# Optimization experiments

Measured on AMD Instinct MI355X. Metric: run time of the kernel, lower is better.

## Reference

```python
import jax, jax.numpy as jnp
import numpy as np
from functools import partial

H = 768          # hidden_size (bert-base)
S = 256          # seq_len, forced by pool Linear(256*H -> H)
V = 30522        # vocab_size
NUM_TAGS = 2
B = 32


def _lstm_layer(x, w_ih, w_hh, b_ih, b_hh):
    # x: (B, S, I); torch weight layout: w_ih (4H, I), w_hh (4H, H), gate order i,f,g,o
    b, _, _ = x.shape
    h0 = jnp.zeros((b, H), x.dtype)
    c0 = jnp.zeros((b, H), x.dtype)
    bias = b_ih + b_hh

    def step(carry, xt):
        h, c = carry
        gates = xt @ w_ih.T + h @ w_hh.T + bias          # (B, 4H)
        i, f, g, o = jnp.split(gates, 4, axis=-1)
        i = jax.nn.sigmoid(i)
        f = jax.nn.sigmoid(f)
        g = jnp.tanh(g)
        o = jax.nn.sigmoid(o)
        c = f * c + i * g
        h = o * jnp.tanh(c)
        return (h, c), h

    _, hs = jax.lax.scan(step, (h0, c0), x.transpose(1, 0, 2))  # hs: (S, B, H)
    return hs.transpose(1, 0, 2)


def setup_inputs() -> dict:
    key = jax.random.key(0)
    ks = jax.random.split(key, 16)
    sc = 0.02
    inp = {
        "input_ids": jax.random.randint(ks[0], (B, S), 0, V, dtype=jnp.int32),
        "attention_mask": jnp.ones((B, S), jnp.int32),
        "token_type_ids": jnp.zeros((B, S), jnp.int32),
        "seq_label": jax.random.randint(ks[1], (B, NUM_TAGS), 0, 2, dtype=jnp.int32),
        "entity_ids": jax.random.randint(ks[2], (B, S), 0, 2, dtype=jnp.int32),
        "embed_table": jax.random.normal(ks[3], (V, H), jnp.float32) * sc,
        "w_ih0": jax.random.normal(ks[4], (4 * H, H), jnp.float32) * sc,
        "w_hh0": jax.random.normal(ks[5], (4 * H, H), jnp.float32) * sc,
        "b_ih0": jnp.zeros((4 * H,), jnp.float32),
        "b_hh0": jnp.zeros((4 * H,), jnp.float32),
        "w_ih1": jax.random.normal(ks[6], (4 * H, H), jnp.float32) * sc,
        "w_hh1": jax.random.normal(ks[7], (4 * H, H), jnp.float32) * sc,
        "b_ih1": jnp.zeros((4 * H,), jnp.float32),
        "b_hh1": jnp.zeros((4 * H,), jnp.float32),
        "pool_w": jax.random.normal(ks[8], (S * H, H), jnp.float32) * 0.002,
        "pool_b": jnp.zeros((H,), jnp.float32),
        "lin_w": jax.random.normal(ks[9], (H, NUM_TAGS), jnp.float32) * sc,
        "lin_b": jnp.zeros((NUM_TAGS,), jnp.float32),
    }
    return inp


def reference(input_ids, attention_mask, token_type_ids, seq_label, entity_ids,
              embed_table, w_ih0, w_hh0, b_ih0, b_hh0, w_ih1, w_hh1, b_ih1, b_hh1,
              pool_w, pool_b, lin_w, lin_b):
    x = embed_table[input_ids]                              # (B, S, H)
    out = _lstm_layer(x, w_ih0, w_hh0, b_ih0, b_hh0)        # layer 1
    out = _lstm_layer(out, w_ih1, w_hh1, b_ih1, b_hh1)      # layer 2 -> (B, S, H)

    seq_out = out.reshape(out.shape[0], -1) @ pool_w + pool_b   # (B, H)

    # batched version of the per-sample loop:
    # entity_out = tokens * (entity_ids == 1); concat seq_out row; global max over tokens
    mask = (entity_ids == 1).astype(out.dtype)[:, :, None]      # (B, S, 1)
    entity_out = out * mask                                     # (B, S, H)
    batch_out = jnp.maximum(entity_out.max(axis=1), seq_out)    # adaptive_max_pool1d(size=1)

    logits = batch_out @ lin_w + lin_b                          # (B, num_tags)

    # BCEWithLogitsLoss (dropout in eval mode = identity), numerically stable
    y = seq_label.astype(logits.dtype)
    loss = jnp.mean(jnp.maximum(logits, 0) - logits * y + jnp.log1p(jnp.exp(-jnp.abs(logits))))
    return (loss, logits)
```

## Files before the change

### kernel.cpp

```cpp
#include <hip/hip_runtime.h>
#include <hip/hip_bf16.h>
#include <stdint.h>

constexpr int Hh  = 768;
constexpr int Ss  = 256;
constexpr int Bb  = 32;
constexpr int G4  = 4 * Hh;
constexpr int MR  = Bb * Ss;
constexpr int NWGL = 96;
constexpr int UPW8 = Hh / NWGL;
constexpr int LCW  = 4 * UPW8;
constexpr int WPAD = Hh + 8;
constexpr int PB   = Bb + 2;
constexpr int KH   = Hh / 2;
constexpr int CPT  = 256;

typedef short bf16x8 __attribute__((ext_vector_type(8)));
typedef float f32x4  __attribute__((ext_vector_type(4)));
typedef float f32x2  __attribute__((ext_vector_type(2)));

__device__ __forceinline__ unsigned short f2bf(float f) {
  union { float f; uint32_t u; } v; v.f = f;
  uint32_t u = v.u;
  return (unsigned short)((u + 0x7FFFu + ((u >> 16) & 1u)) >> 16);
}
__device__ __forceinline__ float bf2f(unsigned short h) {
  union { uint32_t u; float f; } v; v.u = ((uint32_t)h) << 16; return v.f;
}

__global__ __launch_bounds__(256) void k_embed(const int* __restrict__ ids,
                                               const float* __restrict__ table,
                                               unsigned short* __restrict__ x_bf) {
  int row = blockIdx.x;
  int id  = ids[row];
  const float* src = table + (size_t)id * Hh;
  unsigned short* dst = x_bf + (size_t)row * Hh;
  for (int j = threadIdx.x; j < Hh; j += 256) dst[j] = f2bf(src[j]);
}

__global__ __launch_bounds__(256) void k_cast(const float* __restrict__ src,
                                              unsigned short* __restrict__ dst, int n4) {
  int i = blockIdx.x * 256 + threadIdx.x;
  if (i < n4) {
    float4 v = ((const float4*)src)[i];
    uint2 o;
    o.x = (uint32_t)f2bf(v.x) | ((uint32_t)f2bf(v.y) << 16);
    o.y = (uint32_t)f2bf(v.z) | ((uint32_t)f2bf(v.w) << 16);
    ((uint2*)dst)[i] = o;
  }
}

__global__ __launch_bounds__(256) void k_gemm_bt(const unsigned short* __restrict__ A,
                                                 const unsigned short* __restrict__ Bw,
                                                 unsigned short* __restrict__ g2,
                                                 const float* __restrict__ bias1,
                                                 const float* __restrict__ bias2,
                                                 int M, int N, int K) {
  constexpr int BM = 128, BN = 128, BK = 64;
  __shared__ unsigned short Asm[BM * BK];
  __shared__ unsigned short Bsm[BN * BK];
  const int tid = threadIdx.x, lane = tid & 63, wave = tid >> 6;
  const int m0 = blockIdx.x * BM, n0 = blockIdx.y * BN;
  const int wm = (wave & 1) * 64, wn = (wave >> 1) * 64;

  f32x4 acc[4][4];
  #pragma unroll
  for (int a = 0; a < 4; ++a)
    #pragma unroll
    for (int b = 0; b < 4; ++b) acc[a][b] = (f32x4){0.f, 0.f, 0.f, 0.f};

  const int nk = K / BK;
  bf16x8 ar[4], br[4];
  #pragma unroll
  for (int r = 0; r < 4; ++r) {
    int fb = r * 4096 + tid * 16;
    int row = fb >> 7;
    int kb  = (fb >> 4) & 7;
    ar[r] = *(const bf16x8*)(A  + (size_t)(m0 + row) * K + kb * 8);
    br[r] = *(const bf16x8*)(Bw + (size_t)(n0 + row) * K + kb * 8);
  }
  for (int it = 0; it < nk; ++it) {
    __syncthreads();
    #pragma unroll
    for (int r = 0; r < 4; ++r) {
      int fb = r * 4096 + tid * 16;
      int row = fb >> 7;
      int kb  = (fb >> 4) & 7;
      int sb  = kb ^ (row & 7);
      *(bf16x8*)((char*)Asm + row * 128 + sb * 16) = ar[r];
      *(bf16x8*)((char*)Bsm + row * 128 + sb * 16) = br[r];
    }
    __syncthreads();
    if (it + 1 < nk) {
      int k0 = (it + 1) * BK;
      #pragma unroll
      for (int r = 0; r < 4; ++r) {
        int fb = r * 4096 + tid * 16;
        int row = fb >> 7;
        int kb  = (fb >> 4) & 7;
        ar[r] = *(const bf16x8*)(A  + (size_t)(m0 + row) * K + k0 + kb * 8);
        br[r] = *(const bf16x8*)(Bw + (size_t)(n0 + row) * K + k0 + kb * 8);
      }
    }
    #pragma unroll
    for (int kk = 0; kk < 2; ++kk) {
      bf16x8 af[4], bfr[4];
      #pragma unroll
      for (int mi = 0; mi < 4; ++mi) {
        int row = wm + mi * 16 + (lane & 15);
        int kb  = kk * 4 + (lane >> 4);
        int sb  = kb ^ (row & 7);
        af[mi] = *(const bf16x8*)((const char*)Asm + row * 128 + sb * 16);
      }
      #pragma unroll
      for (int ni = 0; ni < 4; ++ni) {
        int row = wn + ni * 16 + (lane & 15);
        int kb  = kk * 4 + (lane >> 4);
        int sb  = kb ^ (row & 7);
        bfr[ni] = *(const bf16x8*)((const char*)Bsm + row * 128 + sb * 16);
      }
      #pragma unroll
      for (int mi = 0; mi < 4; ++mi)
        #pragma unroll
        for (int ni = 0; ni < 4; ++ni)
          acc[mi][ni] = __builtin_amdgcn_mfma_f32_16x16x32_bf16(af[mi], bfr[ni], acc[mi][ni], 0, 0, 0);
    }
  }
  #pragma unroll
  for (int mi = 0; mi < 4; ++mi)
    #pragma unroll
    for (int ni = 0; ni < 4; ++ni)
      #pragma unroll
      for (int r = 0; r < 4; ++r) {
        int row = m0 + wm + mi * 16 + (lane >> 4) * 4 + r;
        int n   = n0 + wn + ni * 16 + (lane & 15);
        int bb = row >> 8, ss = row & 255;
        int gi = n / Hh, u = n - gi * Hh;
        int wg = u >> 3, lc = gi * 8 + (u & 7);
        float v = acc[mi][ni][r] + bias1[n] + bias2[n];
        g2[(((size_t)ss * NWGL + wg) * Bb + bb) * LCW + lc] = f2bf(v);
      }
}

__global__ __launch_bounds__(128) void k_lstm2(
    const unsigned short* __restrict__ g2,
    const unsigned short* __restrict__ w_hh0b,
    const unsigned short* __restrict__ w_ih1b,
    const unsigned short* __restrict__ w_hh1b,
    const float* __restrict__ b_ih1,
    const float* __restrict__ b_hh1,
    unsigned short* __restrict__ hseq1,
    unsigned short* __restrict__ hseq2,
    unsigned int* __restrict__ sync) {
  __shared__ __align__(16) unsigned short Whh[LCW * WPAD];
  __shared__ __align__(16) unsigned short Wih[LCW * WPAD];
  __shared__ __align__(16) unsigned short hbuf[2][16][8];

  const int wgid = blockIdx.x;
  const int tid = threadIdx.x;
  const int lane = tid & 63, w = tid >> 6;
  unsigned int* cnt1 = sync;
  unsigned int* cnt2 = sync + Ss * CPT;

  const int layer = wgid >= NWGL;
  const int wg = layer ? wgid - NWGL : wgid;
  const int u0 = wg * UPW8;
  const int bkt = wg & 15;

  {
    const unsigned short* src = layer ? w_hh1b : w_hh0b;
    for (int cch = tid; cch < LCW * 96; cch += 128) {
      int row = cch / 96, kc = cch - row * 96;
      int gi = row >> 3, u = row & 7;
      *(bf16x8*)&Whh[row * WPAD + kc * 8] =
          *(const bf16x8*)(src + (size_t)(gi * Hh + u0 + u) * Hh + kc * 8);
    }
    if (layer) {
      for (int cch = tid; cch < LCW * 96; cch += 128) {
        int row = cch / 96, kc = cch - row * 96;
        int gi = row >> 3, u = row & 7;
        *(bf16x8*)&Wih[row * WPAD + kc * 8] =
            *(const bf16x8*)(w_ih1b + (size_t)(gi * Hh + u0 + u) * Hh + kc * 8);
      }
    }
  }
  __syncthreads();

  const int l15 = lane & 15, kq = lane >> 4;
  const int brow = w * 16 + l15;
  const bool lo8 = (l15 < 8);

  const float k1 = lo8 ? 2.f : 1.f;
  const float m1 = lo8 ? 2.f : 1.f;
  const float d1 = lo8 ? -1.f : 0.f;

  float bl[2] = {0.f, 0.f};
  if (layer) {
    #pragma unroll
    for (int nt = 0; nt < 2; ++nt) {
      int c = nt * 16 + l15;
      int gcol = (c >> 3) * Hh + u0 + (c & 7);
      bl[nt] = b_ih1[gcol] + b_hh1[gcol];
    }
  }

  unsigned short gc[2][4];
  if (!layer) {
    const unsigned short* grow = g2 + ((size_t)0 * NWGL + wg) * (Bb * LCW);
    #pragma unroll
    for (int nt = 0; nt < 2; ++nt)
      #pragma unroll
      for (int r = 0; r < 4; ++r)
        gc[nt][r] = grow[(w * 16 + kq * 4 + r) * LCW + nt * 16 + l15];
  }
  float cc[4] = {0.f, 0.f, 0.f, 0.f};
  unsigned short* hout = layer ? hseq2 : hseq1;
  unsigned int* mycnt = layer ? cnt2 : cnt1;

  for (int t = 0; t < Ss; ++t) {
    if (layer) {
      if (w == 0) {
        const unsigned int* b1 = cnt1 + (size_t)t * CPT;
        const unsigned int* b2 = cnt2 + (size_t)(t - 1) * CPT;
        const bool needOwn = (t > 0);
        for (;;) {
          unsigned v = 12;
          if (lane < 16)
            v = __hip_atomic_load(b1 + lane * 16, __ATOMIC_RELAXED, __HIP_MEMORY_SCOPE_AGENT);
          else if (lane < 32 && needOwn)
            v = __hip_atomic_load(b2 + (lane - 16) * 16, __ATOMIC_RELAXED, __HIP_MEMORY_SCOPE_AGENT);
          if (__all(v >= 12u)) break;
          __builtin_amdgcn_s_sleep(1);
        }
      }
      __syncthreads();
      asm volatile("" ::: "memory");
    } else if (t > 0) {
      if (w == 0) {
        const unsigned int* b1 = cnt1 + (size_t)(t - 1) * CPT;
        for (;;) {
          unsigned v = 12;
          if (lane < 16)
            v = __hip_atomic_load(b1 + lane * 16, __ATOMIC_RELAXED, __HIP_MEMORY_SCOPE_AGENT);
          if (__all(v >= 12u)) break;
          __builtin_amdgcn_s_sleep(1);
        }
      }
      __syncthreads();
      asm volatile("" ::: "memory");
    }

    f32x4 aI[2][2], aW[2][2];
    #pragma unroll
    for (int nt = 0; nt < 2; ++nt) {
      aI[nt][0] = (f32x4){0.f,0.f,0.f,0.f}; aI[nt][1] = (f32x4){0.f,0.f,0.f,0.f};
      aW[nt][0] = (f32x4){0.f,0.f,0.f,0.f}; aW[nt][1] = (f32x4){0.f,0.f,0.f,0.f};
    }
    if (layer) {
      const unsigned short* ap = hseq1 + ((size_t)t * Bb + brow) * Hh + kq * 8;
      bf16x8 areg[24];
      #pragma unroll
      for (int kk = 0; kk < 24; ++kk) areg[kk] = *(const bf16x8*)(ap + kk * 32);
      #pragma unroll
      for (int nt = 0; nt < 2; ++nt) {
        const int c = nt * 16 + l15;
        #pragma unroll
        for (int kk = 0; kk < 24; ++kk) {
          bf16x8 bfr = *(const bf16x8*)&Wih[c * WPAD + kk * 32 + kq * 8];
          aI[nt][kk & 1] = __builtin_amdgcn_mfma_f32_16x16x32_bf16(areg[kk], bfr, aI[nt][kk & 1], 0, 0, 0);
        }
      }
    }
    if (t > 0) {
      const unsigned short* ap = hout + ((size_t)(t - 1) * Bb + brow) * Hh + kq * 8;
      bf16x8 areg[24];
      #pragma unroll
      for (int kk = 0; kk < 24; ++kk) areg[kk] = *(const bf16x8*)(ap + kk * 32);
      #pragma unroll
      for (int nt = 0; nt < 2; ++nt) {
        const int c = nt * 16 + l15;
        #pragma unroll
        for (int kk = 0; kk < 24; ++kk) {
          bf16x8 bfr = *(const bf16x8*)&Whh[c * WPAD + kk * 32 + kq * 8];
          aW[nt][kk & 1] = __builtin_amdgcn_mfma_f32_16x16x32_bf16(areg[kk], bfr, aW[nt][kk & 1], 0, 0, 0);
        }
      }
    }

    float act0[4], act1[4];
    #pragma unroll
    for (int r = 0; r < 4; ++r) {
      float v0 = aI[0][0][r] + aI[0][1][r] + aW[0][0][r] + aW[0][1][r]
               + (layer ? bl[0] : bf2f(gc[0][r]));
      act0[r] = 1.f / (1.f + __expf(-v0));
      float v1 = aI[1][0][r] + aI[1][1][r] + aW[1][0][r] + aW[1][1][r]
               + (layer ? bl[1] : bf2f(gc[1][r]));
      act1[r] = m1 / (1.f + __expf(-k1 * v1)) + d1;
    }

    #pragma unroll
    for (int r = 0; r < 4; ++r) {
      float p0 = __shfl_xor(act0[r], 8);
      float p1 = __shfl_xor(act1[r], 8);
      float iv = lo8 ? act0[r] : p0;
      float fv = lo8 ? p0 : act0[r];
      float gv = lo8 ? act1[r] : p1;
      float ov = lo8 ? p1 : act1[r];
      float cn = fv * cc[r] + iv * gv;
      cc[r] = cn;
      float e = __expf(-2.f * cn);
      float hv = ov * (1.f - e) / (1.f + e);
      if (lo8) hbuf[w][kq * 4 + r][l15] = f2bf(hv);
    }
    asm volatile("s_waitcnt lgkmcnt(0)" ::: "memory");

    if (lane < 16) {
      const unsigned long long* hb = (const unsigned long long*)&hbuf[w][lane][0];
      unsigned long long x0 = hb[0], x1 = hb[1];
      unsigned long long* hp =
          (unsigned long long*)(hout + ((size_t)t * Bb + (w * 16 + lane)) * Hh + u0);
      __hip_atomic_store(hp + 0, x0, __ATOMIC_RELAXED, __HIP_MEMORY_SCOPE_AGENT);
      __hip_atomic_store(hp + 1, x1, __ATOMIC_RELAXED, __HIP_MEMORY_SCOPE_AGENT);
    }
    asm volatile("s_waitcnt vmcnt(0)" ::: "memory");
    if (lane == 0) {
      unsigned int* cp = mycnt + (size_t)t * CPT + bkt * 16;
      (void)__hip_atomic_fetch_add(cp, 1u, __ATOMIC_RELAXED, __HIP_MEMORY_SCOPE_AGENT);
    }

    if (!layer && t + 1 < Ss) {
      const unsigned short* grow = g2 + ((size_t)(t + 1) * NWGL + wg) * (Bb * LCW);
      #pragma unroll
      for (int nt = 0; nt < 2; ++nt)
        #pragma unroll
        for (int r = 0; r < 4; ++r)
          gc[nt][r] = grow[(w * 16 + kq * 4 + r) * LCW + nt * 16 + l15];
    }
  }
}

__global__ __launch_bounds__(256) void k_pool_partial(const unsigned short* __restrict__ hseq2,
                                                      const float* __restrict__ pw,
                                                      float* __restrict__ partial) {
  __shared__ unsigned short osm[KH * PB];
  const int tid = threadIdx.x;
  const int s = blockIdx.x, half = blockIdx.y;
  const int k0 = half * KH;
  for (int b = 0; b < Bb; ++b) {
    const unsigned short* src = hseq2 + ((size_t)s * Bb + b) * Hh + k0;
    for (int k = tid; k < KH; k += 256) osm[k * PB + b] = src[k];
  }
  __syncthreads();
  f32x2 acc[16][3];
  #pragma unroll
  for (int bp = 0; bp < 16; ++bp)
    #pragma unroll
    for (int j = 0; j < 3; ++j) acc[bp][j] = (f32x2){0.f, 0.f};
  const float* pbase = pw + (size_t)s * Hh * Hh + (size_t)k0 * Hh;
  #pragma unroll 4
  for (int k = 0; k < KH; ++k) {
    float w0 = pbase[(size_t)k * Hh + tid];
    float w1 = pbase[(size_t)k * Hh + 256 + tid];
    float w2 = pbase[(size_t)k * Hh + 512 + tid];
    const uint32_t* orow = (const uint32_t*)&osm[k * PB];
    #pragma unroll
    for (int bp = 0; bp < 16; ++bp) {
      uint32_t pv = orow[bp];
      f32x2 ov;
      ov.x = __uint_as_float(pv << 16);
      ov.y = __uint_as_float(pv & 0xffff0000u);
      acc[bp][0] += ov * w0;
      acc[bp][1] += ov * w1;
      acc[bp][2] += ov * w2;
    }
  }
  float* pout = partial + (size_t)(s * 2 + half) * (Bb * Hh);
  #pragma unroll
  for (int bp = 0; bp < 16; ++bp)
    #pragma unroll
    for (int j = 0; j < 3; ++j) {
      pout[(size_t)(bp * 2 + 0) * Hh + j * 256 + tid] = acc[bp][j].x;
      pout[(size_t)(bp * 2 + 1) * Hh + j * 256 + tid] = acc[bp][j].y;
    }
}

__global__ __launch_bounds__(256) void k_pool_reduce(const float* __restrict__ partial,
                                                     const float* __restrict__ pool_b,
                                                     float* __restrict__ seq_out) {
  int i = blockIdx.x * 256 + threadIdx.x;
  float acc = pool_b[i % Hh];
  #pragma unroll 8
  for (int t = 0; t < 2 * Ss; ++t) acc += partial[(size_t)t * (Bb * Hh) + i];
  seq_out[i] = acc;
}

__global__ __launch_bounds__(256) void k_entity_logits(const unsigned short* __restrict__ hseq2,
                                                       const float* __restrict__ seq_out,
                                                       const int* __restrict__ entity_ids,
                                                       const float* __restrict__ lin_w,
                                                       const float* __restrict__ lin_b,
                                                       float* __restrict__ logits_ws,
                                                       float* __restrict__ dlogits) {
  const int b = blockIdx.x, tid = threadIdx.x;
  float m0 = -1e30f, m1 = -1e30f, m2 = -1e30f;
  for (int s = 0; s < Ss; ++s) {
    bool e = entity_ids[b * Ss + s] == 1;
    const unsigned short* row = hseq2 + ((size_t)s * Bb + b) * Hh;
    float v0 = bf2f(row[tid]);
    float v1 = bf2f(row[256 + tid]);
    float v2 = bf2f(row[512 + tid]);
    v0 = e ? v0 : 0.f; v1 = e ? v1 : 0.f; v2 = e ? v2 : 0.f;
    m0 = fmaxf(m0, v0); m1 = fmaxf(m1, v1); m2 = fmaxf(m2, v2);
  }
  __shared__ float red[512];
  float p0 = 0.f, p1 = 0.f;
  float mm[3] = {m0, m1, m2};
  #pragma unroll
  for (int j = 0; j < 3; ++j) {
    int n = j * 256 + tid;
    float bo = fmaxf(mm[j], seq_out[b * Hh + n]);
    p0 += bo * lin_w[n * 2 + 0];
    p1 += bo * lin_w[n * 2 + 1];
  }
  red[tid] = p0; red[256 + tid] = p1;
  __syncthreads();
  for (int off = 128; off > 0; off >>= 1) {
    if (tid < off) { red[tid] += red[tid + off]; red[256 + tid] += red[256 + tid + off]; }
    __syncthreads();
  }
  if (tid == 0) {
    float l0 = red[0] + lin_b[0], l1 = red[256] + lin_b[1];
    logits_ws[b * 2] = l0; logits_ws[b * 2 + 1] = l1;
    dlogits[b * 2] = l0;  dlogits[b * 2 + 1] = l1;
  }
}

__global__ void k_loss(const float* __restrict__ logits, const int* __restrict__ lab,
                       float* __restrict__ dout) {
  __shared__ float red[64];
  int i = threadIdx.x;
  float l = logits[i];
  float y = (float)lab[i];
  red[i] = fmaxf(l, 0.f) - l * y + log1pf(__expf(-fabsf(l)));
  __syncthreads();
  for (int off = 32; off > 0; off >>= 1) {
    if (i < off) red[i] += red[i + off];
    __syncthreads();
  }
  if (i == 0) dout[0] = red[0] * (1.f / 64.f);
}

extern "C" void kernel_launch(void* const* d_in, const int* in_sizes, int n_in,
                              void* d_out, int out_size, void* d_ws, size_t ws_size,
                              hipStream_t stream) {
  const int*   input_ids  = (const int*)d_in[0];
  const int*   seq_label  = (const int*)d_in[3];
  const int*   entity_ids = (const int*)d_in[4];
  const float* embed      = (const float*)d_in[5];
  const float* w_ih0      = (const float*)d_in[6];
  const float* w_hh0      = (const float*)d_in[7];
  const float* b_ih0      = (const float*)d_in[8];
  const float* b_hh0      = (const float*)d_in[9];
  const float* w_ih1      = (const float*)d_in[10];
  const float* w_hh1      = (const float*)d_in[11];
  const float* b_ih1      = (const float*)d_in[12];
  const float* b_hh1      = (const float*)d_in[13];
  const float* pool_w     = (const float*)d_in[14];
  const float* pool_b     = (const float*)d_in[15];
  const float* lin_w      = (const float*)d_in[16];
  const float* lin_b      = (const float*)d_in[17];
  float* out = (float*)d_out;

  const size_t SZ_XO = (size_t)Bb * Ss * Hh * 2;
  const size_t SZ_W  = (size_t)G4 * Hh * 2;
  const size_t SZ_G  = (size_t)Bb * Ss * G4 * 2;
  const size_t SZ_SY = (size_t)2 * Ss * CPT * 4;
  char* ws = (char*)d_ws;
  size_t off = 0;
  unsigned short* x_bf   = (unsigned short*)(ws + off); off += SZ_XO;
  unsigned short* wb_ih0 = (unsigned short*)(ws + off); off += SZ_W;
  unsigned short* wb_hh0 = (unsigned short*)(ws + off); off += SZ_W;
  unsigned short* wb_ih1 = (unsigned short*)(ws + off); off += SZ_W;
  unsigned short* wb_hh1 = (unsigned short*)(ws + off); off += SZ_W;
  unsigned short* g2     = (unsigned short*)(ws + off); off += SZ_G;
  unsigned short* hseq1  = (unsigned short*)(ws + off); off += SZ_XO;
  unsigned short* hseq2  = (unsigned short*)(ws + off); off += SZ_XO;
  float*          seq_out= (float*)(ws + off);          off += (size_t)Bb * Hh * 4;
  float*          logits = (float*)(ws + off);          off += 1024;
  unsigned int*   syncb  = (unsigned int*)(ws + off);   off += SZ_SY;
  float*          partial = (float*)ws;

  hipMemsetAsync(syncb, 0, SZ_SY, stream);

  k_embed<<<Bb * Ss, 256, 0, stream>>>(input_ids, embed, x_bf);
  int n4 = (G4 * Hh) / 4;
  int cgrid = (n4 + 255) / 256;
  k_cast<<<cgrid, 256, 0, stream>>>(w_ih0, wb_ih0, n4);
  k_cast<<<cgrid, 256, 0, stream>>>(w_hh0, wb_hh0, n4);
  k_cast<<<cgrid, 256, 0, stream>>>(w_ih1, wb_ih1, n4);
  k_cast<<<cgrid, 256, 0, stream>>>(w_hh1, wb_hh1, n4);

  dim3 ggrid(MR / 128, G4 / 128);
  k_gemm_bt<<<ggrid, 256, 0, stream>>>(x_bf, wb_ih0, g2, b_ih0, b_hh0, MR, G4, Hh);

  k_lstm2<<<2 * NWGL, 128, 0, stream>>>(g2, wb_hh0, wb_ih1, wb_hh1,
                                        b_ih1, b_hh1, hseq1, hseq2, syncb);

  dim3 pgrid(Ss, 2);
  k_pool_partial<<<pgrid, 256, 0, stream>>>(hseq2, pool_w, partial);
  k_pool_reduce<<<(Bb * Hh) / 256, 256, 0, stream>>>(partial, pool_b, seq_out);
  k_entity_logits<<<Bb, 256, 0, stream>>>(hseq2, seq_out, entity_ids, lin_w, lin_b,
                                          logits, out + 1);
  k_loss<<<1, 64, 0, stream>>>(logits, seq_label, out);
}
```

Baseline: 2.724 ms.

## Replace counter barriers with sentinel-value polling on hidden-state data

The per-step counter-based cross-workgroup synchronization is removed from the persistent LSTM kernel. Each lane now spins on atomic loads of the hidden-state values it needs, using an all-ones bf16 sentinel (set by memsetting hseq1/hseq2 to 0xFF) to detect unwritten data. This removes the separate counter increments, the vmcnt wait and the workgroup barrier, and overlaps the wait with the operand load itself. The cost is two extra full-buffer memsets, and a genuine 0xFFFF value (a NaN bf16) would cause a hang. The check assumes the two 64-bit halves of a store are seen consistently.

```diff
diff --git a/kernel.cpp b/kernel.cpp
--- a/kernel.cpp
+++ b/kernel.cpp
@@ -13,7 +13,6 @@
 constexpr int WPAD = Hh + 8;
 constexpr int PB   = Bb + 2;
 constexpr int KH   = Hh / 2;
-constexpr int CPT  = 256;
 
 typedef short bf16x8 __attribute__((ext_vector_type(8)));
 typedef float f32x4  __attribute__((ext_vector_type(4)));
@@ -142,6 +141,27 @@
       }
 }
 
+__device__ __forceinline__ void poll_load24(const unsigned short* base,
+                                            unsigned long long (&lo)[24],
+                                            unsigned long long (&hi)[24]) {
+  const unsigned long long* pp = (const unsigned long long*)base;
+  for (;;) {
+    #pragma unroll
+    for (int kk = 0; kk < 24; ++kk) {
+      lo[kk] = __hip_atomic_load(pp + kk * 8,     __ATOMIC_RELAXED, __HIP_MEMORY_SCOPE_AGENT);
+      hi[kk] = __hip_atomic_load(pp + kk * 8 + 1, __ATOMIC_RELAXED, __HIP_MEMORY_SCOPE_AGENT);
+    }
+    bool bad = false;
+    #pragma unroll
+    for (int kk = 0; kk < 24; ++kk) {
+      bad = bad || (((unsigned)lo[kk] & 0xFFFFu) == 0xFFFFu);
+      bad = bad || (((unsigned)hi[kk] & 0xFFFFu) == 0xFFFFu);
+    }
+    if (__all(!bad)) return;
+    __builtin_amdgcn_s_sleep(1);
+  }
+}
+
 __global__ __launch_bounds__(128) void k_lstm2(
     const unsigned short* __restrict__ g2,
     const unsigned short* __restrict__ w_hh0b,
@@ -150,8 +170,7 @@
     const float* __restrict__ b_ih1,
     const float* __restrict__ b_hh1,
     unsigned short* __restrict__ hseq1,
-    unsigned short* __restrict__ hseq2,
-    unsigned int* __restrict__ sync) {
+    unsigned short* __restrict__ hseq2) {
   __shared__ __align__(16) unsigned short Whh[LCW * WPAD];
   __shared__ __align__(16) unsigned short Wih[LCW * WPAD];
   __shared__ __align__(16) unsigned short hbuf[2][16][8];
@@ -159,13 +178,10 @@
   const int wgid = blockIdx.x;
   const int tid = threadIdx.x;
   const int lane = tid & 63, w = tid >> 6;
-  unsigned int* cnt1 = sync;
-  unsigned int* cnt2 = sync + Ss * CPT;
 
   const int layer = wgid >= NWGL;
   const int wg = layer ? wgid - NWGL : wgid;
   const int u0 = wg * UPW8;
-  const int bkt = wg & 15;
 
   {
     const unsigned short* src = layer ? w_hh1b : w_hh0b;
@@ -215,74 +231,42 @@
   }
   float cc[4] = {0.f, 0.f, 0.f, 0.f};
   unsigned short* hout = layer ? hseq2 : hseq1;
-  unsigned int* mycnt = layer ? cnt2 : cnt1;
+
+  unsigned long long alo[24], ahi[24];
 
   for (int t = 0; t < Ss; ++t) {
-    if (layer) {
-      if (w == 0) {
-        const unsigned int* b1 = cnt1 + (size_t)t * CPT;
-        const unsigned int* b2 = cnt2 + (size_t)(t - 1) * CPT;
-        const bool needOwn = (t > 0);
-        for (;;) {
-          unsigned v = 12;
-          if (lane < 16)
-            v = __hip_atomic_load(b1 + lane * 16, __ATOMIC_RELAXED, __HIP_MEMORY_SCOPE_AGENT);
-          else if (lane < 32 && needOwn)
-            v = __hip_atomic_load(b2 + (lane - 16) * 16, __ATOMIC_RELAXED, __HIP_MEMORY_SCOPE_AGENT);
-          if (__all(v >= 12u)) break;
-          __builtin_amdgcn_s_sleep(1);
-        }
-      }
-      __syncthreads();
-      asm volatile("" ::: "memory");
-    } else if (t > 0) {
-      if (w == 0) {
-        const unsigned int* b1 = cnt1 + (size_t)(t - 1) * CPT;
-        for (;;) {
-          unsigned v = 12;
-          if (lane < 16)
-            v = __hip_atomic_load(b1 + lane * 16, __ATOMIC_RELAXED, __HIP_MEMORY_SCOPE_AGENT);
-          if (__all(v >= 12u)) break;
-          __builtin_amdgcn_s_sleep(1);
-        }
-      }
-      __syncthreads();
-      asm volatile("" ::: "memory");
-    }
-
-    f32x4 aI[2][2], aW[2][2];
+    f32x4 aW[2][2], aI[2][2];
     #pragma unroll
     for (int nt = 0; nt < 2; ++nt) {
+      aW[nt][0] = (f32x4){0.f,0.f,0.f,0.f}; aW[nt][1] = (f32x4){0.f,0.f,0.f,0.f};
       aI[nt][0] = (f32x4){0.f,0.f,0.f,0.f}; aI[nt][1] = (f32x4){0.f,0.f,0.f,0.f};
-      aW[nt][0] = (f32x4){0.f,0.f,0.f,0.f}; aW[nt][1] = (f32x4){0.f,0.f,0.f,0.f};
-    }
-    if (layer) {
-      const unsigned short* ap = hseq1 + ((size_t)t * Bb + brow) * Hh + kq * 8;
-      bf16x8 areg[24];
-      #pragma unroll
-      for (int kk = 0; kk < 24; ++kk) areg[kk] = *(const bf16x8*)(ap + kk * 32);
+    }
+
+    if (t > 0) {
+      poll_load24(hout + ((size_t)(t - 1) * Bb + brow) * Hh + kq * 8, alo, ahi);
       #pragma unroll
       for (int nt = 0; nt < 2; ++nt) {
         const int c = nt * 16 + l15;
         #pragma unroll
         for (int kk = 0; kk < 24; ++kk) {
-          bf16x8 bfr = *(const bf16x8*)&Wih[c * WPAD + kk * 32 + kq * 8];
-          aI[nt][kk & 1] = __builtin_amdgcn_mfma_f32_16x16x32_bf16(areg[kk], bfr, aI[nt][kk & 1], 0, 0, 0);
+          union { unsigned long long q[2]; bf16x8 v; } u;
+          u.q[0] = alo[kk]; u.q[1] = ahi[kk];
+          bf16x8 bfr = *(const bf16x8*)&Whh[c * WPAD + kk * 32 + kq * 8];
+          aW[nt][kk & 1] = __builtin_amdgcn_mfma_f32_16x16x32_bf16(u.v, bfr, aW[nt][kk & 1], 0, 0, 0);
         }
       }
     }
-    if (t > 0) {
-      const unsigned short* ap = hout + ((size_t)(t - 1) * Bb + brow) * Hh + kq * 8;
-      bf16x8 areg[24];
-      #pragma unroll
-      for (int kk = 0; kk < 24; ++kk) areg[kk] = *(const bf16x8*)(ap + kk * 32);
+    if (layer) {
+      poll_load24(hseq1 + ((size_t)t * Bb + brow) * Hh + kq * 8, alo, ahi);
       #pragma unroll
       for (int nt = 0; nt < 2; ++nt) {
         const int c = nt * 16 + l15;
         #pragma unroll
         for (int kk = 0; kk < 24; ++kk) {
-          bf16x8 bfr = *(const bf16x8*)&Whh[c * WPAD + kk * 32 + kq * 8];
-          aW[nt][kk & 1] = __builtin_amdgcn_mfma_f32_16x16x32_bf16(areg[kk], bfr, aW[nt][kk & 1], 0, 0, 0);
+          union { unsigned long long q[2]; bf16x8 v; } u;
+          u.q[0] = alo[kk]; u.q[1] = ahi[kk];
+          bf16x8 bfr = *(const bf16x8*)&Wih[c * WPAD + kk * 32 + kq * 8];
+          aI[nt][kk & 1] = __builtin_amdgcn_mfma_f32_16x16x32_bf16(u.v, bfr, aI[nt][kk & 1], 0, 0, 0);
         }
       }
     }
@@ -290,10 +274,10 @@
     float act0[4], act1[4];
     #pragma unroll
     for (int r = 0; r < 4; ++r) {
-      float v0 = aI[0][0][r] + aI[0][1][r] + aW[0][0][r] + aW[0][1][r]
+      float v0 = aW[0][0][r] + aW[0][1][r] + aI[0][0][r] + aI[0][1][r]
                + (layer ? bl[0] : bf2f(gc[0][r]));
       act0[r] = 1.f / (1.f + __expf(-v0));
-      float v1 = aI[1][0][r] + aI[1][1][r] + aW[1][0][r] + aW[1][1][r]
+      float v1 = aW[1][0][r] + aW[1][1][r] + aI[1][0][r] + aI[1][1][r]
                + (layer ? bl[1] : bf2f(gc[1][r]));
       act1[r] = m1 / (1.f + __expf(-k1 * v1)) + d1;
     }
@@ -321,11 +305,6 @@
           (unsigned long long*)(hout + ((size_t)t * Bb + (w * 16 + lane)) * Hh + u0);
       __hip_atomic_store(hp + 0, x0, __ATOMIC_RELAXED, __HIP_MEMORY_SCOPE_AGENT);
       __hip_atomic_store(hp + 1, x1, __ATOMIC_RELAXED, __HIP_MEMORY_SCOPE_AGENT);
-    }
-    asm volatile("s_waitcnt vmcnt(0)" ::: "memory");
-    if (lane == 0) {
-      unsigned int* cp = mycnt + (size_t)t * CPT + bkt * 16;
-      (void)__hip_atomic_fetch_add(cp, 1u, __ATOMIC_RELAXED, __HIP_MEMORY_SCOPE_AGENT);
     }
 
     if (!layer && t + 1 < Ss) {
@@ -474,7 +453,6 @@
   const size_t SZ_XO = (size_t)Bb * Ss * Hh * 2;
   const size_t SZ_W  = (size_t)G4 * Hh * 2;
   const size_t SZ_G  = (size_t)Bb * Ss * G4 * 2;
-  const size_t SZ_SY = (size_t)2 * Ss * CPT * 4;
   char* ws = (char*)d_ws;
   size_t off = 0;
   unsigned short* x_bf   = (unsigned short*)(ws + off); off += SZ_XO;
@@ -487,10 +465,10 @@
   unsigned short* hseq2  = (unsigned short*)(ws + off); off += SZ_XO;
   float*          seq_out= (float*)(ws + off);          off += (size_t)Bb * Hh * 4;
   float*          logits = (float*)(ws + off);          off += 1024;
-  unsigned int*   syncb  = (unsigned int*)(ws + off);   off += SZ_SY;
   float*          partial = (float*)ws;
 
-  hipMemsetAsync(syncb, 0, SZ_SY, stream);
+  hipMemsetAsync(hseq1, 0xFF, SZ_XO, stream);
+  hipMemsetAsync(hseq2, 0xFF, SZ_XO, stream);
 
   k_embed<<<Bb * Ss, 256, 0, stream>>>(input_ids, embed, x_bf);
   int n4 = (G4 * Hh) / 4;
@@ -504,7 +482,7 @@
   k_gemm_bt<<<ggrid, 256, 0, stream>>>(x_bf, wb_ih0, g2, b_ih0, b_hh0, MR, G4, Hh);
 
   k_lstm2<<<2 * NWGL, 128, 0, stream>>>(g2, wb_hh0, wb_ih1, wb_hh1,
-                                        b_ih1, b_hh1, hseq1, hseq2, syncb);
+                                        b_ih1, b_hh1, hseq1, hseq2);
 
   dim3 pgrid(Ss, 2);
   k_pool_partial<<<pgrid, 256, 0, stream>>>(hseq2, pool_w, partial);
```

Result: slower. 4.491 ms (+64.9%).
